# Kernel optimization log

Hardware: AMD Instinct MI355X
Metric: run time of the kernel (lower is better)

Reference implementation:

```python
import jax, jax.numpy as jnp
import numpy as np

N = 50000   # nodes (WSI patches)
G = 8       # graphs in batch
E = 400000  # edges (k-NN patch graph)
D = 512     # in_channels
HC = 512    # hidden_channels (fixed by Linear(512,*) in pooling)
OUT = 1     # out_channels (binary, sigmoid+squeeze)


def segment_softmax(e, idx, num_segments):
    m = jax.ops.segment_max(e, idx, num_segments=num_segments)
    m = jnp.where(jnp.isfinite(m), m, 0.0)
    ex = jnp.exp(e - m[idx])
    s = jax.ops.segment_sum(ex, idx, num_segments=num_segments)
    return ex / (s[idx] + 1e-16)


def setup_inputs() -> dict:
    key = jax.random.key(0)
    ks = jax.random.split(key, 16)
    x = jax.random.normal(ks[0], (N, D), jnp.float32)
    src = jax.random.randint(ks[1], (E,), 0, N)
    dst = jax.random.randint(ks[2], (E,), 0, N)
    edge_index = jnp.stack([src, dst]).astype(jnp.int64)
    batch = jnp.sort(jax.random.randint(ks[3], (N,), 0, G)).astype(jnp.int64)
    sc = 1.0 / np.sqrt(D).astype(np.float32)
    return {
        "x": x,
        "edge_index": edge_index,
        "batch": batch,
        # GATConv (heads=1, concat=True defaults)
        "W": jax.random.normal(ks[4], (D, HC), jnp.float32) * sc,
        "att_src": jax.random.normal(ks[5], (HC,), jnp.float32) * sc,
        "att_dst": jax.random.normal(ks[6], (HC,), jnp.float32) * sc,
        "b_conv": jnp.zeros((HC,), jnp.float32),
        # AttentionalAggregation: gate_nn = Linear(512,1), nn = Linear(512,512)
        "Wg": jax.random.normal(ks[7], (HC, 1), jnp.float32) * sc,
        "bg": jnp.zeros((1,), jnp.float32),
        "Wn": jax.random.normal(ks[8], (HC, HC), jnp.float32) * sc,
        "bn": jnp.zeros((HC,), jnp.float32),
        # classifier head
        "W1": jax.random.normal(ks[9], (HC, HC), jnp.float32) * sc,
        "b1": jnp.zeros((HC,), jnp.float32),
        "W2": jax.random.normal(ks[10], (HC, OUT), jnp.float32) * sc,
        "b2": jnp.zeros((OUT,), jnp.float32),
    }


def reference(x, edge_index, batch, W, att_src, att_dst, b_conv,
              Wg, bg, Wn, bn, W1, b1, W2, b2):
    # ---- GATConv (heads=1): linear, per-edge attention, segment softmax ----
    h = x @ W  # [N, HC]
    loops = jnp.arange(N, dtype=edge_index.dtype)
    src = jnp.concatenate([edge_index[0], loops])  # add_self_loops=True
    dst = jnp.concatenate([edge_index[1], loops])
    a_s = h @ att_src  # [N]
    a_d = h @ att_dst  # [N]
    e = jax.nn.leaky_relu(a_s[src] + a_d[dst], 0.2)     # [E+N]
    alpha = segment_softmax(e, dst, N)                  # softmax over incoming edges
    hconv = jax.ops.segment_sum(alpha[:, None] * h[src], dst, num_segments=N)
    hconv = hconv + b_conv  # [N, HC]
    # (Dropout omitted: deterministic eval reference)

    # ---- AttentionalAggregation over batch index ----
    gate = hconv @ Wg + bg                 # [N, 1]
    xn = hconv @ Wn + bn                   # [N, HC]
    g = segment_softmax(gate[:, 0], batch, G)[:, None]  # [N, 1]
    pooled = jax.ops.segment_sum(g * xn, batch, num_segments=G)  # [G, HC]

    # ---- classifier head ----
    out = jax.nn.relu(pooled @ W1 + b1)
    out = jnp.squeeze(jax.nn.sigmoid(out @ W2 + b2))  # [G]
    return out, g
```

## Files before the change

### kernel.cpp

```cpp
#include <hip/hip_runtime.h>
#include <stdint.h>

#define N_NODES 50000
#define N_PAD   50048
#define GQ      8
#define EE      400000
#define DIM     512
#define NE_TOT  450000
#define NBLK_SCAN 196

typedef __attribute__((ext_vector_type(8))) __bf16 bf16x8;
typedef __attribute__((ext_vector_type(4))) float f32x4;

__device__ __forceinline__ float bf2f(unsigned short u){ return __uint_as_float(((unsigned)u) << 16); }
__device__ __forceinline__ unsigned short f2bf(float f){
  unsigned u = __float_as_uint(f);
  return (unsigned short)((u + 0x7fffu + ((u >> 16) & 1u)) >> 16);
}
__device__ __forceinline__ unsigned pk2(float lo, float hi){
  return (unsigned)f2bf(lo) | ((unsigned)f2bf(hi) << 16);
}
__device__ __forceinline__ float dot4(float4 a, float4 b){ return a.x*b.x + a.y*b.y + a.z*b.z + a.w*b.w; }
__device__ __forceinline__ float wredSum(float v){
#pragma unroll
  for (int o = 32; o > 0; o >>= 1) v += __shfl_xor(v, o, 64);
  return v;
}
__device__ __forceinline__ int wredSumI(int v){
#pragma unroll
  for (int o = 32; o > 0; o >>= 1) v += __shfl_xor(v, o, 64);
  return v;
}
__device__ __forceinline__ float wredMax(float v){
#pragma unroll
  for (int o = 32; o > 0; o >>= 1) v = fmaxf(v, __shfl_xor(v, o, 64));
  return v;
}
__device__ __forceinline__ void gload_lds16(const void* g, void* l){
  __builtin_amdgcn_global_load_lds((__attribute__((address_space(1))) void*)g,
                                   (__attribute__((address_space(3))) void*)l, 16, 0, 0);
}
__device__ __forceinline__ void consume8(float* ac, uint4 u, float al){
  ac[0] += al * bf2f((unsigned short)u.x); ac[1] += al * bf2f((unsigned short)(u.x >> 16));
  ac[2] += al * bf2f((unsigned short)u.y); ac[3] += al * bf2f((unsigned short)(u.y >> 16));
  ac[4] += al * bf2f((unsigned short)u.z); ac[5] += al * bf2f((unsigned short)(u.z >> 16));
  ac[6] += al * bf2f((unsigned short)u.w); ac[7] += al * bf2f((unsigned short)(u.w >> 16));
}

static constexpr size_t AL(size_t x){ return (x + 255) & ~(size_t)255; }
static constexpr size_t OFF_XBF   = 0;
static constexpr size_t OFF_HBF   = OFF_XBF   + AL((size_t)N_PAD * DIM * 2);
static constexpr size_t OFF_HCONV = OFF_HBF   + AL((size_t)N_PAD * DIM * 2);
static constexpr size_t OFF_WTBF  = OFF_HCONV + AL((size_t)N_NODES * DIM * 2);
static constexpr size_t OFF_WNT   = OFF_WTBF  + AL((size_t)DIM * DIM * 2);
static constexpr size_t OFF_W1T   = OFF_WNT   + AL((size_t)DIM * DIM * 4);
static constexpr size_t OFF_WSS   = OFF_W1T   + AL((size_t)DIM * DIM * 4);
static constexpr size_t OFF_WSD   = OFF_WSS   + AL((size_t)DIM * 4);
static constexpr size_t OFF_AS    = OFF_WSD   + AL((size_t)DIM * 4);
static constexpr size_t OFF_AD    = OFF_AS    + AL((size_t)N_NODES * 4);
static constexpr size_t OFF_GATE  = OFF_AD    + AL((size_t)N_NODES * 4);
static constexpr size_t OFF_CNT   = OFF_GATE  + AL((size_t)N_NODES * 4);
static constexpr size_t OFF_FILL  = OFF_CNT   + AL((size_t)N_NODES * 4);
static constexpr size_t OFF_RS    = OFF_FILL  + AL((size_t)N_NODES * 4);
static constexpr size_t OFF_CSR   = OFF_RS    + AL((size_t)(N_NODES + 1) * 4);
static constexpr size_t OFF_BSUM  = OFF_CSR   + AL((size_t)NE_TOT * 4);
static constexpr size_t OFF_GSUM  = OFF_BSUM  + AL((size_t)NBLK_SCAN * 4);
static constexpr size_t OFF_PP    = OFF_GSUM  + AL((size_t)GQ * 4);
static constexpr size_t OFF_POOL  = OFF_PP    + AL((size_t)GQ * DIM * 4);
static constexpr size_t OFF_Z1    = OFF_POOL  + AL((size_t)GQ * DIM * 4);


__global__ void k_setup(const float* __restrict__ W, const float* __restrict__ atS,
                        const float* __restrict__ atD, const float* __restrict__ Wn,
                        const float* __restrict__ W1,
                        float* ws_s, float* ws_d,
                        unsigned short* __restrict__ WtBf, float* __restrict__ WnT,
                        float* __restrict__ W1T,
                        int* cnt, int* fill, float* gsum, float* pp){
  __shared__ float tile[64][65];
  int bx = blockIdx.x;
  if (bx < NBLK_SCAN){
    int i = bx * 256 + threadIdx.x;
    if (i < N_NODES){ cnt[i] = 1; fill[i] = 0; }
    if (i < GQ) gsum[i] = 0.f;
    if (i < GQ * DIM) pp[i] = 0.f;
    if (bx < 128){
      int wid = threadIdx.x >> 6, lane = threadIdx.x & 63;
      int k = bx * 4 + wid;
      const float4* row = (const float4*)(W + (size_t)k * DIM);
      float4 r0 = row[lane * 2], r1 = row[lane * 2 + 1];
      const float4* s4 = (const float4*)atS;
      const float4* d4 = (const float4*)atD;
      float vs = dot4(r0, s4[lane * 2]) + dot4(r1, s4[lane * 2 + 1]);
      float vd = dot4(r0, d4[lane * 2]) + dot4(r1, d4[lane * 2 + 1]);
      vs = wredSum(vs); vd = wredSum(vd);
      if (lane == 0){ ws_s[k] = vs; ws_d[k] = vd; }
    }
  } else {
    int tb = bx - NBLK_SCAN;
    int y = tb >> 6, bq = tb & 63;
    const float* src = (y == 0) ? W : (y == 1) ? Wn : W1;
    int bi = bq & 7, bj = bq >> 3;
    int r0 = bi * 64, c0 = bj * 64;
#pragma unroll
    for (int ii = 0; ii < 16; ++ii){
      int idx = ii * 256 + threadIdx.x;
      int r = idx >> 6, c = idx & 63;
      tile[r][c] = src[(size_t)(r0 + r) * DIM + c0 + c];
    }
    __syncthreads();
#pragma unroll
    for (int ii = 0; ii < 16; ++ii){
      int idx = ii * 256 + threadIdx.x;
      int cc = idx >> 6, rr = idx & 63;
      float v = tile[rr][cc];
      size_t o = (size_t)(c0 + cc) * DIM + r0 + rr;
      if (y == 0) WtBf[o] = f2bf(v);
      else if (y == 1) WnT[o] = v;
      else W1T[o] = v;
    }
  }
}

__global__ __launch_bounds__(256) void k_cast(const float* __restrict__ x,
                                              const float* __restrict__ ws_s,
                                              const float* __restrict__ ws_d,
                                              const int* __restrict__ ei, int* cnt,
                                              unsigned short* __restrict__ x_bf,
                                              float* __restrict__ a_s, float* __restrict__ a_d){
  int gt = blockIdx.x * 256 + threadIdx.x;
  if (gt < EE) atomicAdd(&cnt[ei[EE + gt]], 1);
  int wid = threadIdx.x >> 6, lane = threadIdx.x & 63;
  size_t i = (size_t)blockIdx.x * 4 + wid;
  if (i >= N_PAD) return;
  unsigned short* orow = x_bf + i * DIM;
  if (i >= N_NODES){
    ((uint4*)orow)[lane] = make_uint4(0, 0, 0, 0);
    return;
  }
  const float4* xr = (const float4*)(x + i * DIM);
  float4 v0 = xr[lane * 2], v1 = xr[lane * 2 + 1];
  ((uint4*)orow)[lane] = make_uint4(pk2(v0.x, v0.y), pk2(v0.z, v0.w), pk2(v1.x, v1.y), pk2(v1.z, v1.w));
  const float4* s4 = (const float4*)ws_s;
  const float4* d4 = (const float4*)ws_d;
  float vs = dot4(v0, s4[lane * 2]) + dot4(v1, s4[lane * 2 + 1]);
  float vd = dot4(v0, d4[lane * 2]) + dot4(v1, d4[lane * 2 + 1]);
  vs = wredSum(vs); vd = wredSum(vd);
  if (lane == 0){ a_s[i] = vs; a_d[i] = vd; }
}

__global__ __launch_bounds__(256, 2) void k_gemm(const unsigned short* __restrict__ A,
                                                 const unsigned short* __restrict__ Bt,
                                                 unsigned short* __restrict__ H){
  __shared__ unsigned short As[128 * 32];
  __shared__ unsigned short Bs[256 * 32];
  const int tid = threadIdx.x;
  const int wid = tid >> 6, lane = tid & 63, quad = lane >> 4, l16 = lane & 15;
  const int m0 = blockIdx.x * 128, n0 = blockIdx.y * 256;
  const int wm = (wid & 1) * 64, wn = (wid >> 1) * 128;
  const int qa = quad ^ ((l16 >> 1) & 3);
  f32x4 acc[4][8] = {};
  for (int kt = 0; kt < 16; ++kt){
    const int k0 = kt * 32;
    __syncthreads();
#pragma unroll
    for (int r = 0; r < 2; ++r){
      int p = r * 256 + tid;
      int mm = p >> 2;
      int qg = (p & 3) ^ ((mm >> 1) & 3);
      gload_lds16(A + (size_t)(m0 + mm) * DIM + k0 + qg * 8,
                  As + (size_t)(r * 256 + wid * 64) * 8);
    }
#pragma unroll
    for (int r = 0; r < 4; ++r){
      int p = r * 256 + tid;
      int mm = p >> 2;
      int qg = (p & 3) ^ ((mm >> 1) & 3);
      gload_lds16(Bt + (size_t)(n0 + mm) * DIM + k0 + qg * 8,
                  Bs + (size_t)(r * 256 + wid * 64) * 8);
    }
    __syncthreads();
    bf16x8 af[4], bfr[8];
#pragma unroll
    for (int f = 0; f < 4; ++f)
      af[f]  = *(const bf16x8*)(As + (wm + f * 16 + l16) * 32 + qa * 8);
#pragma unroll
    for (int f = 0; f < 8; ++f)
      bfr[f] = *(const bf16x8*)(Bs + (wn + f * 16 + l16) * 32 + qa * 8);
#pragma unroll
    for (int fm = 0; fm < 4; ++fm)
#pragma unroll
      for (int fn = 0; fn < 8; ++fn)
        acc[fm][fn] = __builtin_amdgcn_mfma_f32_16x16x32_bf16(af[fm], bfr[fn], acc[fm][fn], 0, 0, 0);
  }
#pragma unroll
  for (int fm = 0; fm < 4; ++fm){
#pragma unroll
    for (int r = 0; r < 4; ++r){
      size_t gro = (size_t)(m0 + wm + fm * 16 + quad * 4 + r) * DIM + n0 + wn + l16;
#pragma unroll
      for (int fn = 0; fn < 8; ++fn)
        H[gro + fn * 16] = f2bf(acc[fm][fn][r]);
    }
  }
}

__global__ void k_scanA(const int* __restrict__ cnt, int* rs, int* bsum){
  __shared__ int sm[256];
  int t = threadIdx.x, i = blockIdx.x * 256 + t;
  int v = (i < N_NODES) ? cnt[i] : 0;
  sm[t] = v; __syncthreads();
#pragma unroll
  for (int off = 1; off < 256; off <<= 1){
    int nv = (t >= off) ? sm[t - off] : 0;
    __syncthreads();
    sm[t] += nv;
    __syncthreads();
  }
  if (i < N_NODES) rs[i] = sm[t] - v;
  if (t == 255) bsum[blockIdx.x] = sm[255];
}

__global__ void k_scanC_fill(int* rs, const int* __restrict__ bsum, int* csr){
  __shared__ int sm4[4];
  int t = threadIdx.x;
  int acc = 0;
  for (int k = t; k < blockIdx.x; k += 256) acc += bsum[k];
  acc = wredSumI(acc);
  if ((t & 63) == 0) sm4[t >> 6] = acc;
  __syncthreads();
  int boff = sm4[0] + sm4[1] + sm4[2] + sm4[3];
  int i = blockIdx.x * 256 + t;
  if (i < N_NODES){
    int v = rs[i] + boff;
    rs[i] = v;
    csr[v] = i;
  }
  if (i == 0) rs[N_NODES] = NE_TOT;
}

__global__ void k_fill_edges(const int* __restrict__ ei, const int* __restrict__ rs,
                             int* fill, int* csr){
  int e = blockIdx.x * 256 + threadIdx.x;
  if (e < EE){
    int s = ei[e], d = ei[EE + e];
    int p = atomicAdd(&fill[d], 1);
    csr[rs[d] + 1 + p] = s;
  }
}

__global__ __launch_bounds__(256) void k_edge(const int* __restrict__ rs, const int* __restrict__ csr,
                                              const float* __restrict__ a_s, const float* __restrict__ a_d,
                                              const unsigned short* __restrict__ h_bf,
                                              const float* __restrict__ bconv,
                                              const float* __restrict__ Wg, const float* __restrict__ bg,
                                              unsigned short* __restrict__ hconv, float* __restrict__ gate){
  int wid = threadIdx.x >> 6, lane = threadIdx.x & 63;
  int i = blockIdx.x * 4 + wid;
  if (i >= N_NODES) return;
  int r0 = rs[i], r1 = rs[i + 1];
  int deg = r1 - r0;
  float adi = a_d[i];
  float ac[8] = {0.f, 0.f, 0.f, 0.f, 0.f, 0.f, 0.f, 0.f};

  if (deg <= 128){
    int s_l0 = 0, s_l1 = 0;
    float e_a = -__builtin_inff(), e_b = -__builtin_inff();
    if (lane < deg){ s_l0 = csr[r0 + lane]; float e = a_s[s_l0] + adi; e_a = (e > 0.f) ? e : 0.2f * e; }
    if (64 + lane < deg){ s_l1 = csr[r0 + 64 + lane]; float e = a_s[s_l1] + adi; e_b = (e > 0.f) ? e : 0.2f * e; }
    float mx = wredMax(fmaxf(e_a, e_b));
    float x0 = (lane < deg) ? __expf(e_a - mx) : 0.f;
    float x1 = (64 + lane < deg) ? __expf(e_b - mx) : 0.f;
    float inv = 1.f / (wredSum(x0 + x1) + 1e-16f);

    auto FETCH = [&](int jj, uint4& u, float& al){
      int s  = __shfl((jj < 64) ? s_l0 : s_l1, jj & 63);
      al = __shfl((jj < 64) ? x0 : x1, jj & 63) * inv;
      u = *((const uint4*)(h_bf + (size_t)s * DIM) + lane);
    };
    uint4 u0, u1, u2, u3; float f0, f1, f2, f3;
    if (deg > 0) FETCH(0, u0, f0);
    if (deg > 1) FETCH(1, u1, f1);
    if (deg > 2) FETCH(2, u2, f2);
    if (deg > 3) FETCH(3, u3, f3);
    for (int j = 0; j < deg; j += 4){
      consume8(ac, u0, f0); if (j + 4 < deg) FETCH(j + 4, u0, f0);
      if (j + 1 >= deg) break;
      consume8(ac, u1, f1); if (j + 5 < deg) FETCH(j + 5, u1, f1);
      if (j + 2 >= deg) break;
      consume8(ac, u2, f2); if (j + 6 < deg) FETCH(j + 6, u2, f2);
      if (j + 3 >= deg) break;
      consume8(ac, u3, f3); if (j + 7 < deg) FETCH(j + 7, u3, f3);
    }
  } else {
    float mx = -__builtin_inff();
    for (int j = r0 + lane; j < r1; j += 64){
      float e = a_s[csr[j]] + adi; e = (e > 0.f) ? e : 0.2f * e;
      mx = fmaxf(mx, e);
    }
    mx = wredMax(mx);
    float ssum = 0.f;
    for (int j = r0 + lane; j < r1; j += 64){
      float e = a_s[csr[j]] + adi; e = (e > 0.f) ? e : 0.2f * e;
      ssum += __expf(e - mx);
    }
    float inv = 1.f / (wredSum(ssum) + 1e-16f);
    for (int j = r0; j < r1; ++j){
      int s = csr[j];
      float e = a_s[s] + adi; e = (e > 0.f) ? e : 0.2f * e;
      float al = __expf(e - mx) * inv;
      uint4 u = *((const uint4*)(h_bf + (size_t)s * DIM) + lane);
      consume8(ac, u, al);
    }
  }

  float4 bc0 = ((const float4*)bconv)[lane * 2];
  float4 bc1 = ((const float4*)bconv)[lane * 2 + 1];
  ac[0] += bc0.x; ac[1] += bc0.y; ac[2] += bc0.z; ac[3] += bc0.w;
  ac[4] += bc1.x; ac[5] += bc1.y; ac[6] += bc1.z; ac[7] += bc1.w;
  ((uint4*)(hconv + (size_t)i * DIM))[lane] =
      make_uint4(pk2(ac[0], ac[1]), pk2(ac[2], ac[3]), pk2(ac[4], ac[5]), pk2(ac[6], ac[7]));
  float4 w0 = ((const float4*)Wg)[lane * 2];
  float4 w1 = ((const float4*)Wg)[lane * 2 + 1];
  float gp = ac[0]*w0.x + ac[1]*w0.y + ac[2]*w0.z + ac[3]*w0.w
           + ac[4]*w1.x + ac[5]*w1.y + ac[6]*w1.z + ac[7]*w1.w;
  gp = wredSum(gp);
  if (lane == 0) gate[i] = gp + bg[0];
}

__global__ void k_gsum(const float* __restrict__ gate, const int* __restrict__ batch, float* gsum){
  __shared__ float sm[GQ];
  int t = threadIdx.x, i = blockIdx.x * 512 + t;
  if (t < GQ) sm[t] = 0.f;
  __syncthreads();
  if (i < N_NODES) atomicAdd(&sm[batch[i]], __expf(gate[i]));
  __syncthreads();
  if (t < GQ && sm[t] != 0.f) atomicAdd(&gsum[t], sm[t]);
}

__global__ __launch_bounds__(256) void k_pool(const unsigned short* __restrict__ hconv,
                                              const int* __restrict__ batch,
                                              const float* __restrict__ gate,
                                              const float* __restrict__ gsum,
                                              float* __restrict__ out_g, float* pp){
  __shared__ float gv_s[128];
  __shared__ int b_s[128];
  int t = threadIdx.x;
  int base = blockIdx.x * 128;
  if (t < 128){
    int i = base + t;
    if (i < N_NODES){
      int b = batch[i];
      float gv = __expf(gate[i]) / (gsum[b] + 1e-16f);
      gv_s[t] = gv; b_s[t] = b;
      out_g[i] = gv;
    } else { gv_s[t] = 0.f; b_s[t] = -1; }
  }
  __syncthreads();
  int lim = N_NODES - base; if (lim > 128) lim = 128;
  float ax = 0.f, ay = 0.f;
  int cur = b_s[0];
#pragma unroll 4
  for (int r = 0; r < lim; ++r){
    int b = b_s[r];
    float gv = gv_s[r];
    if (b != cur){
      atomicAdd(&pp[cur * DIM + 2 * t], ax);
      atomicAdd(&pp[cur * DIM + 2 * t + 1], ay);
      ax = ay = 0.f; cur = b;
    }
    unsigned u = *(const unsigned*)(hconv + (size_t)(base + r) * DIM + 2 * t);
    ax += gv * bf2f((unsigned short)(u & 0xffffu));
    ay += gv * bf2f((unsigned short)(u >> 16));
  }
  if (cur >= 0){
    atomicAdd(&pp[cur * DIM + 2 * t], ax);
    atomicAdd(&pp[cur * DIM + 2 * t + 1], ay);
  }
}

template<bool RELU>
__global__ void k_headA(const float* __restrict__ src, const float* __restrict__ WT,
                        const float* __restrict__ bias, float* dst){
  __shared__ float sp[GQ * DIM];
  int t = threadIdx.x;
  for (int idx = t; idx < GQ * DIM; idx += 256) sp[idx] = src[idx];
  __syncthreads();
  int wid = t >> 6, lane = t & 63;
  int j = blockIdx.x * 4 + wid;
  const float4* wr = (const float4*)(WT + (size_t)j * DIM);
  float4 w0 = wr[lane * 2], w1 = wr[lane * 2 + 1];
  float bj = bias[j];
#pragma unroll
  for (int g = 0; g < GQ; ++g){
    const float* pg = sp + g * DIM + lane * 8;
    float s = w0.x*pg[0] + w0.y*pg[1] + w0.z*pg[2] + w0.w*pg[3]
            + w1.x*pg[4] + w1.y*pg[5] + w1.z*pg[6] + w1.w*pg[7];
    s = wredSum(s);
    if (lane == 0){
      s += bj;
      if (RELU) s = fmaxf(s, 0.f);
      dst[g * DIM + j] = s;
    }
  }
}

__global__ void k_headC(const float* __restrict__ z1, const float* __restrict__ W2,
                        const float* __restrict__ b2, float* __restrict__ out){
  int wv = threadIdx.x >> 6, lane = threadIdx.x & 63;
  const float4* zr = (const float4*)(z1 + (size_t)wv * DIM);
  const float4* w4 = (const float4*)W2;
  float s = dot4(zr[lane * 2], w4[lane * 2]) + dot4(zr[lane * 2 + 1], w4[lane * 2 + 1]);
  s = wredSum(s);
  if (lane == 0) out[wv] = 1.f / (1.f + __expf(-(s + b2[0])));
}

extern "C" void kernel_launch(void* const* d_in, const int* in_sizes, int n_in,
                              void* d_out, int out_size, void* d_ws, size_t ws_size,
                              hipStream_t stream){
  (void)in_sizes; (void)n_in; (void)out_size; (void)ws_size;
  const float* x   = (const float*)d_in[0];
  const int*   ei  = (const int*)d_in[1];
  const int*   bat = (const int*)d_in[2];
  const float* W   = (const float*)d_in[3];
  const float* atS = (const float*)d_in[4];
  const float* atD = (const float*)d_in[5];
  const float* bcv = (const float*)d_in[6];
  const float* Wg  = (const float*)d_in[7];
  const float* bg  = (const float*)d_in[8];
  const float* Wn  = (const float*)d_in[9];
  const float* bn  = (const float*)d_in[10];
  const float* W1  = (const float*)d_in[11];
  const float* b1  = (const float*)d_in[12];
  const float* W2  = (const float*)d_in[13];
  const float* b2  = (const float*)d_in[14];
  float* out = (float*)d_out;
  char* ws = (char*)d_ws;

  unsigned short* x_bf  = (unsigned short*)(ws + OFF_XBF);
  unsigned short* h_bf  = (unsigned short*)(ws + OFF_HBF);
  unsigned short* hconv = (unsigned short*)(ws + OFF_HCONV);
  unsigned short* Wt_bf = (unsigned short*)(ws + OFF_WTBF);
  float* WnT  = (float*)(ws + OFF_WNT);
  float* W1T  = (float*)(ws + OFF_W1T);
  float* ws_s = (float*)(ws + OFF_WSS);
  float* ws_d = (float*)(ws + OFF_WSD);
  float* a_s  = (float*)(ws + OFF_AS);
  float* a_d  = (float*)(ws + OFF_AD);
  float* gate = (float*)(ws + OFF_GATE);
  int* cnt  = (int*)(ws + OFF_CNT);
  int* fill = (int*)(ws + OFF_FILL);
  int* rs   = (int*)(ws + OFF_RS);
  int* csr  = (int*)(ws + OFF_CSR);
  int* bsum = (int*)(ws + OFF_BSUM);
  float* gsum = (float*)(ws + OFF_GSUM);
  float* pp   = (float*)(ws + OFF_PP);
  float* pool = (float*)(ws + OFF_POOL);
  float* z1   = (float*)(ws + OFF_Z1);

  hipLaunchKernelGGL(k_setup, dim3(NBLK_SCAN + 192), dim3(256), 0, stream,
                     W, atS, atD, Wn, W1, ws_s, ws_d, Wt_bf, WnT, W1T, cnt, fill, gsum, pp);
  hipLaunchKernelGGL(k_cast, dim3(N_PAD / 4), dim3(256), 0, stream,
                     x, ws_s, ws_d, ei, cnt, x_bf, a_s, a_d);
  hipLaunchKernelGGL(k_gemm, dim3(N_PAD / 128, 2), dim3(256), 0, stream, x_bf, Wt_bf, h_bf);
  hipLaunchKernelGGL(k_scanA, dim3(NBLK_SCAN), dim3(256), 0, stream, cnt, rs, bsum);
  hipLaunchKernelGGL(k_scanC_fill, dim3(NBLK_SCAN), dim3(256), 0, stream, rs, bsum, csr);
  hipLaunchKernelGGL(k_fill_edges, dim3((EE + 255) / 256), dim3(256), 0, stream, ei, rs, fill, csr);
  hipLaunchKernelGGL(k_edge, dim3(N_NODES / 4), dim3(256), 0, stream,
                     rs, csr, a_s, a_d, h_bf, bcv, Wg, bg, hconv, gate);
  hipLaunchKernelGGL(k_gsum, dim3(98), dim3(512), 0, stream, gate, bat, gsum);
  hipLaunchKernelGGL(k_pool, dim3((N_NODES + 127) / 128), dim3(256), 0, stream,
                     hconv, bat, gate, gsum, out + GQ, pp);
  hipLaunchKernelGGL((k_headA<false>), dim3(128), dim3(256), 0, stream, pp, WnT, bn, pool);
  hipLaunchKernelGGL((k_headA<true>),  dim3(128), dim3(256), 0, stream, pool, W1T, b1, z1);
  hipLaunchKernelGGL(k_headC, dim3(1), dim3(512), 0, stream, z1, W2, b2, out);
}
```

Baseline: 394.5 us.

## Store node features in FP8 and pack source attention scores into CSR

```diff
diff --git a/kernel.cpp b/kernel.cpp
--- a/kernel.cpp
+++ b/kernel.cpp
@@ -40,18 +40,25 @@
   __builtin_amdgcn_global_load_lds((__attribute__((address_space(1))) void*)g,
                                    (__attribute__((address_space(3))) void*)l, 16, 0, 0);
 }
-__device__ __forceinline__ void consume8(float* ac, uint4 u, float al){
-  ac[0] += al * bf2f((unsigned short)u.x); ac[1] += al * bf2f((unsigned short)(u.x >> 16));
-  ac[2] += al * bf2f((unsigned short)u.y); ac[3] += al * bf2f((unsigned short)(u.y >> 16));
-  ac[4] += al * bf2f((unsigned short)u.z); ac[5] += al * bf2f((unsigned short)(u.z >> 16));
-  ac[6] += al * bf2f((unsigned short)u.w); ac[7] += al * bf2f((unsigned short)(u.w >> 16));
+__device__ __forceinline__ unsigned char f2fp8(float x){
+  return (unsigned char)__builtin_amdgcn_cvt_pk_fp8_f32(x, x, 0, false);
+}
+__device__ __forceinline__ void consumeF8(float* ac, uint2 u, float al){
+  auto p0 = __builtin_amdgcn_cvt_pk_f32_fp8(u.x, false);
+  auto p1 = __builtin_amdgcn_cvt_pk_f32_fp8(u.x, true);
+  auto p2 = __builtin_amdgcn_cvt_pk_f32_fp8(u.y, false);
+  auto p3 = __builtin_amdgcn_cvt_pk_f32_fp8(u.y, true);
+  ac[0] += al * p0[0]; ac[1] += al * p0[1];
+  ac[2] += al * p1[0]; ac[3] += al * p1[1];
+  ac[4] += al * p2[0]; ac[5] += al * p2[1];
+  ac[6] += al * p3[0]; ac[7] += al * p3[1];
 }
 
 static constexpr size_t AL(size_t x){ return (x + 255) & ~(size_t)255; }
 static constexpr size_t OFF_XBF   = 0;
-static constexpr size_t OFF_HBF   = OFF_XBF   + AL((size_t)N_PAD * DIM * 2);
-static constexpr size_t OFF_HCONV = OFF_HBF   + AL((size_t)N_PAD * DIM * 2);
-static constexpr size_t OFF_WTBF  = OFF_HCONV + AL((size_t)N_NODES * DIM * 2);
+static constexpr size_t OFF_HF8   = OFF_XBF   + AL((size_t)N_PAD * DIM * 2);
+static constexpr size_t OFF_HCV8  = OFF_HF8   + AL((size_t)N_PAD * DIM);
+static constexpr size_t OFF_WTBF  = OFF_HCV8  + AL((size_t)N_NODES * DIM);
 static constexpr size_t OFF_WNT   = OFF_WTBF  + AL((size_t)DIM * DIM * 2);
 static constexpr size_t OFF_W1T   = OFF_WNT   + AL((size_t)DIM * DIM * 4);
 static constexpr size_t OFF_WSS   = OFF_W1T   + AL((size_t)DIM * DIM * 4);
@@ -62,8 +69,8 @@
 static constexpr size_t OFF_CNT   = OFF_GATE  + AL((size_t)N_NODES * 4);
 static constexpr size_t OFF_FILL  = OFF_CNT   + AL((size_t)N_NODES * 4);
 static constexpr size_t OFF_RS    = OFF_FILL  + AL((size_t)N_NODES * 4);
-static constexpr size_t OFF_CSR   = OFF_RS    + AL((size_t)(N_NODES + 1) * 4);
-static constexpr size_t OFF_BSUM  = OFF_CSR   + AL((size_t)NE_TOT * 4);
+static constexpr size_t OFF_CSR2  = OFF_RS    + AL((size_t)(N_NODES + 1) * 4);
+static constexpr size_t OFF_BSUM  = OFF_CSR2  + AL((size_t)NE_TOT * 8);
 static constexpr size_t OFF_GSUM  = OFF_BSUM  + AL((size_t)NBLK_SCAN * 4);
 static constexpr size_t OFF_PP    = OFF_GSUM  + AL((size_t)GQ * 4);
 static constexpr size_t OFF_POOL  = OFF_PP    + AL((size_t)GQ * DIM * 4);
@@ -151,7 +158,7 @@
 
 __global__ __launch_bounds__(256, 2) void k_gemm(const unsigned short* __restrict__ A,
                                                  const unsigned short* __restrict__ Bt,
-                                                 unsigned short* __restrict__ H){
+                                                 unsigned char* __restrict__ H8){
   __shared__ unsigned short As[128 * 32];
   __shared__ unsigned short Bs[256 * 32];
   const int tid = threadIdx.x;
@@ -200,7 +207,7 @@
       size_t gro = (size_t)(m0 + wm + fm * 16 + quad * 4 + r) * DIM + n0 + wn + l16;
 #pragma unroll
       for (int fn = 0; fn < 8; ++fn)
-        H[gro + fn * 16] = f2bf(acc[fm][fn][r]);
+        H8[gro + fn * 16] = f2fp8(acc[fm][fn][r]);
     }
   }
 }
@@ -221,7 +228,8 @@
   if (t == 255) bsum[blockIdx.x] = sm[255];
 }
 
-__global__ void k_scanC_fill(int* rs, const int* __restrict__ bsum, int* csr){
+__global__ void k_scanC_fill(int* rs, const int* __restrict__ bsum,
+                             const float* __restrict__ a_s, int2* csr2){
   __shared__ int sm4[4];
   int t = threadIdx.x;
   int acc = 0;
@@ -234,27 +242,27 @@
   if (i < N_NODES){
     int v = rs[i] + boff;
     rs[i] = v;
-    csr[v] = i;
+    csr2[v] = make_int2(i, __float_as_int(a_s[i]));
   }
   if (i == 0) rs[N_NODES] = NE_TOT;
 }
 
 __global__ void k_fill_edges(const int* __restrict__ ei, const int* __restrict__ rs,
-                             int* fill, int* csr){
+                             const float* __restrict__ a_s, int* fill, int2* csr2){
   int e = blockIdx.x * 256 + threadIdx.x;
   if (e < EE){
     int s = ei[e], d = ei[EE + e];
     int p = atomicAdd(&fill[d], 1);
-    csr[rs[d] + 1 + p] = s;
-  }
-}
-
-__global__ __launch_bounds__(256) void k_edge(const int* __restrict__ rs, const int* __restrict__ csr,
-                                              const float* __restrict__ a_s, const float* __restrict__ a_d,
-                                              const unsigned short* __restrict__ h_bf,
+    csr2[rs[d] + 1 + p] = make_int2(s, __float_as_int(a_s[s]));
+  }
+}
+
+__global__ __launch_bounds__(256) void k_edge(const int* __restrict__ rs, const int2* __restrict__ csr2,
+                                              const float* __restrict__ a_d,
+                                              const unsigned char* __restrict__ h8,
                                               const float* __restrict__ bconv,
                                               const float* __restrict__ Wg, const float* __restrict__ bg,
-                                              unsigned short* __restrict__ hconv, float* __restrict__ gate){
+                                              unsigned char* __restrict__ hconv8, float* __restrict__ gate){
   int wid = threadIdx.x >> 6, lane = threadIdx.x & 63;
   int i = blockIdx.x * 4 + wid;
   if (i >= N_NODES) return;
@@ -266,51 +274,70 @@
   if (deg <= 128){
     int s_l0 = 0, s_l1 = 0;
     float e_a = -__builtin_inff(), e_b = -__builtin_inff();
-    if (lane < deg){ s_l0 = csr[r0 + lane]; float e = a_s[s_l0] + adi; e_a = (e > 0.f) ? e : 0.2f * e; }
-    if (64 + lane < deg){ s_l1 = csr[r0 + 64 + lane]; float e = a_s[s_l1] + adi; e_b = (e > 0.f) ? e : 0.2f * e; }
+    if (lane < deg){
+      int2 c = csr2[r0 + lane]; s_l0 = c.x;
+      float e = __int_as_float(c.y) + adi; e_a = (e > 0.f) ? e : 0.2f * e;
+    }
+    if (64 + lane < deg){
+      int2 c = csr2[r0 + 64 + lane]; s_l1 = c.x;
+      float e = __int_as_float(c.y) + adi; e_b = (e > 0.f) ? e : 0.2f * e;
+    }
     float mx = wredMax(fmaxf(e_a, e_b));
     float x0 = (lane < deg) ? __expf(e_a - mx) : 0.f;
     float x1 = (64 + lane < deg) ? __expf(e_b - mx) : 0.f;
     float inv = 1.f / (wredSum(x0 + x1) + 1e-16f);
 
-    auto FETCH = [&](int jj, uint4& u, float& al){
+    auto FETCH = [&](int jj, uint2& u, float& al){
       int s  = __shfl((jj < 64) ? s_l0 : s_l1, jj & 63);
       al = __shfl((jj < 64) ? x0 : x1, jj & 63) * inv;
-      u = *((const uint4*)(h_bf + (size_t)s * DIM) + lane);
+      u = *((const uint2*)(h8 + (size_t)s * DIM) + lane);
     };
-    uint4 u0, u1, u2, u3; float f0, f1, f2, f3;
+    uint2 u0, u1, u2, u3, u4, u5, u6, u7;
+    float f0, f1, f2, f3, f4, f5, f6, f7;
     if (deg > 0) FETCH(0, u0, f0);
     if (deg > 1) FETCH(1, u1, f1);
     if (deg > 2) FETCH(2, u2, f2);
     if (deg > 3) FETCH(3, u3, f3);
-    for (int j = 0; j < deg; j += 4){
-      consume8(ac, u0, f0); if (j + 4 < deg) FETCH(j + 4, u0, f0);
+    if (deg > 4) FETCH(4, u4, f4);
+    if (deg > 5) FETCH(5, u5, f5);
+    if (deg > 6) FETCH(6, u6, f6);
+    if (deg > 7) FETCH(7, u7, f7);
+    for (int j = 0; j < deg; j += 8){
+      consumeF8(ac, u0, f0); if (j + 8  < deg) FETCH(j + 8,  u0, f0);
       if (j + 1 >= deg) break;
-      consume8(ac, u1, f1); if (j + 5 < deg) FETCH(j + 5, u1, f1);
+      consumeF8(ac, u1, f1); if (j + 9  < deg) FETCH(j + 9,  u1, f1);
       if (j + 2 >= deg) break;
-      consume8(ac, u2, f2); if (j + 6 < deg) FETCH(j + 6, u2, f2);
+      consumeF8(ac, u2, f2); if (j + 10 < deg) FETCH(j + 10, u2, f2);
       if (j + 3 >= deg) break;
-      consume8(ac, u3, f3); if (j + 7 < deg) FETCH(j + 7, u3, f3);
+      consumeF8(ac, u3, f3); if (j + 11 < deg) FETCH(j + 11, u3, f3);
+      if (j + 4 >= deg) break;
+      consumeF8(ac, u4, f4); if (j + 12 < deg) FETCH(j + 12, u4, f4);
+      if (j + 5 >= deg) break;
+      consumeF8(ac, u5, f5); if (j + 13 < deg) FETCH(j + 13, u5, f5);
+      if (j + 6 >= deg) break;
+      consumeF8(ac, u6, f6); if (j + 14 < deg) FETCH(j + 14, u6, f6);
+      if (j + 7 >= deg) break;
+      consumeF8(ac, u7, f7); if (j + 15 < deg) FETCH(j + 15, u7, f7);
     }
   } else {
     float mx = -__builtin_inff();
     for (int j = r0 + lane; j < r1; j += 64){
-      float e = a_s[csr[j]] + adi; e = (e > 0.f) ? e : 0.2f * e;
+      float e = __int_as_float(csr2[j].y) + adi; e = (e > 0.f) ? e : 0.2f * e;
       mx = fmaxf(mx, e);
     }
     mx = wredMax(mx);
     float ssum = 0.f;
     for (int j = r0 + lane; j < r1; j += 64){
-      float e = a_s[csr[j]] + adi; e = (e > 0.f) ? e : 0.2f * e;
+      float e = __int_as_float(csr2[j].y) + adi; e = (e > 0.f) ? e : 0.2f * e;
       ssum += __expf(e - mx);
     }
     float inv = 1.f / (wredSum(ssum) + 1e-16f);
     for (int j = r0; j < r1; ++j){
-      int s = csr[j];
-      float e = a_s[s] + adi; e = (e > 0.f) ? e : 0.2f * e;
+      int2 c = csr2[j];
+      float e = __int_as_float(c.y) + adi; e = (e > 0.f) ? e : 0.2f * e;
       float al = __expf(e - mx) * inv;
-      uint4 u = *((const uint4*)(h_bf + (size_t)s * DIM) + lane);
-      consume8(ac, u, al);
+      uint2 u = *((const uint2*)(h8 + (size_t)c.x * DIM) + lane);
+      consumeF8(ac, u, al);
     }
   }
 
@@ -318,12 +345,15 @@
   float4 bc1 = ((const float4*)bconv)[lane * 2 + 1];
   ac[0] += bc0.x; ac[1] += bc0.y; ac[2] += bc0.z; ac[3] += bc0.w;
   ac[4] += bc1.x; ac[5] += bc1.y; ac[6] += bc1.z; ac[7] += bc1.w;
-  ((uint4*)(hconv + (size_t)i * DIM))[lane] =
-      make_uint4(pk2(ac[0], ac[1]), pk2(ac[2], ac[3]), pk2(ac[4], ac[5]), pk2(ac[6], ac[7]));
-  float4 w0 = ((const float4*)Wg)[lane * 2];
-  float4 w1 = ((const float4*)Wg)[lane * 2 + 1];
-  float gp = ac[0]*w0.x + ac[1]*w0.y + ac[2]*w0.z + ac[3]*w0.w
-           + ac[4]*w1.x + ac[5]*w1.y + ac[6]*w1.z + ac[7]*w1.w;
+  unsigned w0 = (unsigned)__builtin_amdgcn_cvt_pk_fp8_f32(ac[0], ac[1], 0, false);
+  w0 = (unsigned)__builtin_amdgcn_cvt_pk_fp8_f32(ac[2], ac[3], (int)w0, true);
+  unsigned w1 = (unsigned)__builtin_amdgcn_cvt_pk_fp8_f32(ac[4], ac[5], 0, false);
+  w1 = (unsigned)__builtin_amdgcn_cvt_pk_fp8_f32(ac[6], ac[7], (int)w1, true);
+  ((uint2*)(hconv8 + (size_t)i * DIM))[lane] = make_uint2(w0, w1);
+  float4 wg0 = ((const float4*)Wg)[lane * 2];
+  float4 wg1 = ((const float4*)Wg)[lane * 2 + 1];
+  float gp = ac[0]*wg0.x + ac[1]*wg0.y + ac[2]*wg0.z + ac[3]*wg0.w
+           + ac[4]*wg1.x + ac[5]*wg1.y + ac[6]*wg1.z + ac[7]*wg1.w;
   gp = wredSum(gp);
   if (lane == 0) gate[i] = gp + bg[0];
 }
@@ -338,7 +368,7 @@
   if (t < GQ && sm[t] != 0.f) atomicAdd(&gsum[t], sm[t]);
 }
 
-__global__ __launch_bounds__(256) void k_pool(const unsigned short* __restrict__ hconv,
+__global__ __launch_bounds__(256) void k_pool(const unsigned char* __restrict__ hconv8,
                                               const int* __restrict__ batch,
                                               const float* __restrict__ gate,
                                               const float* __restrict__ gsum,
@@ -369,9 +399,10 @@
       atomicAdd(&pp[cur * DIM + 2 * t + 1], ay);
       ax = ay = 0.f; cur = b;
     }
-    unsigned u = *(const unsigned*)(hconv + (size_t)(base + r) * DIM + 2 * t);
-    ax += gv * bf2f((unsigned short)(u & 0xffffu));
-    ay += gv * bf2f((unsigned short)(u >> 16));
+    unsigned us = *(const unsigned short*)(hconv8 + (size_t)(base + r) * DIM + 2 * t);
+    auto p = __builtin_amdgcn_cvt_pk_f32_fp8(us, false);
+    ax += gv * p[0];
+    ay += gv * p[1];
   }
   if (cur >= 0){
     atomicAdd(&pp[cur * DIM + 2 * t], ax);
@@ -437,10 +468,10 @@
   float* out = (float*)d_out;
   char* ws = (char*)d_ws;
 
-  unsigned short* x_bf  = (unsigned short*)(ws + OFF_XBF);
-  unsigned short* h_bf  = (unsigned short*)(ws + OFF_HBF);
-  unsigned short* hconv = (unsigned short*)(ws + OFF_HCONV);
-  unsigned short* Wt_bf = (unsigned short*)(ws + OFF_WTBF);
+  unsigned short* x_bf   = (unsigned short*)(ws + OFF_XBF);
+  unsigned char*  h8     = (unsigned char*)(ws + OFF_HF8);
+  unsigned char*  hconv8 = (unsigned char*)(ws + OFF_HCV8);
+  unsigned short* Wt_bf  = (unsigned short*)(ws + OFF_WTBF);
   float* WnT  = (float*)(ws + OFF_WNT);
   float* W1T  = (float*)(ws + OFF_W1T);
   float* ws_s = (float*)(ws + OFF_WSS);
@@ -451,7 +482,7 @@
   int* cnt  = (int*)(ws + OFF_CNT);
   int* fill = (int*)(ws + OFF_FILL);
   int* rs   = (int*)(ws + OFF_RS);
-  int* csr  = (int*)(ws + OFF_CSR);
+  int2* csr2 = (int2*)(ws + OFF_CSR2);
   int* bsum = (int*)(ws + OFF_BSUM);
   float* gsum = (float*)(ws + OFF_GSUM);
   float* pp   = (float*)(ws + OFF_PP);
@@ -462,15 +493,15 @@
                      W, atS, atD, Wn, W1, ws_s, ws_d, Wt_bf, WnT, W1T, cnt, fill, gsum, pp);
   hipLaunchKernelGGL(k_cast, dim3(N_PAD / 4), dim3(256), 0, stream,
                      x, ws_s, ws_d, ei, cnt, x_bf, a_s, a_d);
-  hipLaunchKernelGGL(k_gemm, dim3(N_PAD / 128, 2), dim3(256), 0, stream, x_bf, Wt_bf, h_bf);
+  hipLaunchKernelGGL(k_gemm, dim3(N_PAD / 128, 2), dim3(256), 0, stream, x_bf, Wt_bf, h8);
   hipLaunchKernelGGL(k_scanA, dim3(NBLK_SCAN), dim3(256), 0, stream, cnt, rs, bsum);
-  hipLaunchKernelGGL(k_scanC_fill, dim3(NBLK_SCAN), dim3(256), 0, stream, rs, bsum, csr);
-  hipLaunchKernelGGL(k_fill_edges, dim3((EE + 255) / 256), dim3(256), 0, stream, ei, rs, fill, csr);
+  hipLaunchKernelGGL(k_scanC_fill, dim3(NBLK_SCAN), dim3(256), 0, stream, rs, bsum, a_s, csr2);
+  hipLaunchKernelGGL(k_fill_edges, dim3((EE + 255) / 256), dim3(256), 0, stream, ei, rs, a_s, fill, csr2);
   hipLaunchKernelGGL(k_edge, dim3(N_NODES / 4), dim3(256), 0, stream,
-                     rs, csr, a_s, a_d, h_bf, bcv, Wg, bg, hconv, gate);
+                     rs, csr2, a_d, h8, bcv, Wg, bg, hconv8, gate);
   hipLaunchKernelGGL(k_gsum, dim3(98), dim3(512), 0, stream, gate, bat, gsum);
   hipLaunchKernelGGL(k_pool, dim3((N_NODES + 127) / 128), dim3(256), 0, stream,
-                     hconv, bat, gate, gsum, out + GQ, pp);
+                     hconv8, bat, gate, gsum, out + GQ, pp);
   hipLaunchKernelGGL((k_headA<false>), dim3(128), dim3(256), 0, stream, pp, WnT, bn, pool);
   hipLaunchKernelGGL((k_headA<true>),  dim3(128), dim3(256), 0, stream, pool, W1T, b1, z1);
   hipLaunchKernelGGL(k_headC, dim3(1), dim3(512), 0, stream, z1, W2, b2, out);
```

Result: faster. 380.0 us (-3.7%).
